# Kernel tuning notes

Measured on AMD Instinct MI355X. Metric: run time of the kernel, lower is better.

## Reference

```python
import jax, jax.numpy as jnp
import numpy as np

TAU = 0.3  # default tau in selectCom_adap
K = 1      # hard-coded K in selectCom_adap

B, C, N, M = 8, 64, 2048, 2048


def setup_inputs() -> dict:
    key = jax.random.key(0)
    k1, k2, k3, k4 = jax.random.split(key, 4)
    return {
        "src_emb": jax.random.normal(k1, (B, C, N), dtype=jnp.float32),
        "tgt_emb": jax.random.normal(k2, (B, C, M), dtype=jnp.float32),
        "src": jax.random.normal(k3, (B, 3, N), dtype=jnp.float32),
        "tgt": jax.random.normal(k4, (B, 3, M), dtype=jnp.float32),
    }


def reference(src_emb, tgt_emb, src, tgt):
    # EPCOR eval path: selectCom_adap + get_sparse_w
    dtype = src_emb.dtype
    Np = src_emb.shape[2]
    Mp = tgt_emb.shape[2]
    tgt_K = int(Mp * TAU)
    src_K = int(Np * TAU)

    inner = jnp.einsum('bcn,bcm->bnm', src_emb, tgt_emb)
    xx = jnp.sum(src_emb * src_emb, axis=1)[:, :, None]   # [B,N,1]
    yy = jnp.sum(tgt_emb * tgt_emb, axis=1)[:, None, :]   # [B,1,M]
    pd = 2.0 * inner - xx - yy                             # [B,N,M]

    # column softmax and tgt outlier mask (smallest tgt_K column mass)
    scoresSoftCol = jax.nn.softmax(pd, axis=2)
    scoresColSum = jnp.sum(scoresSoftCol, axis=1)          # [B,M]
    col_thresh = -jax.lax.top_k(-scoresColSum, tgt_K)[0][:, -1]  # tgt_K-th smallest, [B]
    mask_tgt = (scoresColSum < col_thresh[:, None])[:, None, :]  # [B,1,M]

    # row softmax and src outlier mask (smallest src_K row mass)
    scoresSoftRow = jax.nn.softmax(pd, axis=1)
    scoresRowSum = jnp.sum(scoresSoftRow, axis=2)          # [B,N]
    row_thresh = -jax.lax.top_k(-scoresRowSum, src_K)[0][:, -1]  # [B]
    mask_src = (scoresRowSum < row_thresh[:, None])[:, :, None]  # [B,N,1]

    mask = jnp.logical_or(mask_src, mask_tgt)              # [B,N,M]

    # torch precedence: mask = (mask + scoresSoftCol) < topk  (bool promoted to float)
    topk = jax.lax.top_k(scoresSoftCol, K)[0][..., -1:]    # K-th largest per row, [B,N,1]
    mask = (mask.astype(dtype) + scoresSoftCol) < topk     # [B,N,M]

    w_sparse = jnp.where(mask, jnp.zeros((), dtype), scoresSoftCol)
    colsum = jnp.sum(w_sparse, axis=-1, keepdims=True)
    colsum = jnp.where(colsum < 1e-5, jnp.asarray(1e-5, dtype), colsum)
    src_tgt_weight = w_sparse / colsum                     # row-renormalized sparse weights

    val_sum = jnp.sum(src_tgt_weight, axis=-1, keepdims=True)  # [B,N,1]
    val_sum_inlier = jnp.where(mask_src, jnp.zeros((), dtype), val_sum)[..., 0]  # [B,N]
    src_weight = val_sum_inlier / jnp.sum(val_sum_inlier, axis=-1, keepdims=True)

    # src_corr = tgt @ src_tgt_weight^T : [B,3,M] x [B,N,M] -> [B,3,N]
    src_corr = jnp.einsum('bdm,bnm->bdn', tgt, src_tgt_weight)
    return src_corr, src_weight, mask_src, mask_tgt
```

## Files before the change

### kernel.cpp

```cpp
#include <hip/hip_runtime.h>

#define BB 8
#define CC 64
#define NN 2048
#define MM 2048
#define KSEL 613
#define MT 32
#define MT2 16
#define NT2 16
#define NCH 16

#define OUT_W  (BB * 3 * NN)
#define OUT_MS (OUT_W + BB * NN)
#define OUT_MT (OUT_MS + BB * NN)

typedef __bf16 bf16x8 __attribute__((ext_vector_type(8)));
typedef float f32x4 __attribute__((ext_vector_type(4)));
typedef unsigned short u16;

#define MFMA16 __builtin_amdgcn_mfma_f32_16x16x32_bf16

__device__ __forceinline__ void split3(float a, u16& u0, u16& u1, u16& u2) {
    __bf16 h0 = (__bf16)a; float f0 = (float)h0;
    float r1 = a - f0;
    __bf16 h1 = (__bf16)r1; float f1 = (float)h1;
    float r2 = r1 - f1;
    __bf16 h2 = (__bf16)r2;
    u0 = __builtin_bit_cast(u16, h0);
    u1 = __builtin_bit_cast(u16, h1);
    u2 = __builtin_bit_cast(u16, h2);
}

__global__ __launch_bounds__(256) void split_k(const float* __restrict__ E,
                                               float* __restrict__ sq,
                                               unsigned* __restrict__ T0,
                                               unsigned* __restrict__ T1,
                                               unsigned* __restrict__ T2) {
    __shared__ float Ls[64][65];
    __shared__ float sacc[64];
    int b = blockIdx.y, n0 = blockIdx.x * 64, t = threadIdx.x;
    const float* Eb = E + (size_t)b * CC * NN + n0;
#pragma unroll
    for (int i = 0; i < 4; ++i) {
        int idx = (i << 8) + t, c = idx >> 4, nq = idx & 15;
        float4 v = *(const float4*)(Eb + (size_t)c * NN + (nq << 2));
        Ls[c][nq * 4 + 0] = v.x; Ls[c][nq * 4 + 1] = v.y;
        Ls[c][nq * 4 + 2] = v.z; Ls[c][nq * 4 + 3] = v.w;
    }
    __syncthreads();
    int j = t & 31, nn = t >> 5;
#pragma unroll
    for (int p = 0; p < 8; ++p) {
        int n = (p << 3) + nn;
        float a = Ls[2 * j][n], c = Ls[2 * j + 1][n];
        float s = a * a + c * c;
#pragma unroll
        for (int d = 1; d < 32; d <<= 1) s += __shfl_xor(s, d);
        if (j == 0) sacc[n] = s;
        u16 a0, a1, a2, c0, c1, c2;
        split3(a, a0, a1, a2);
        split3(c, c0, c1, c2);
        size_t row = (size_t)(b * NN + n0 + n) * 32 + j;
        T0[row] = (unsigned)a0 | ((unsigned)c0 << 16);
        T1[row] = (unsigned)a1 | ((unsigned)c1 << 16);
        T2[row] = (unsigned)a2 | ((unsigned)c2 << 16);
    }
    __syncthreads();
    if (t < 64) sq[b * NN + n0 + t] = sacc[t];
}

__device__ __forceinline__ void stage_tile(u16* dst, const unsigned* src,
                                           int base_nm, int kc, int t) {
#pragma unroll
    for (int i = 0; i < 2; ++i) {
        int d = (((i << 8) + t) << 4);
        int nn_ = d >> 6, c4 = (d >> 4) & 3;
        const char* gs = (const char*)src + ((size_t)(base_nm + nn_) << 7) +
                         ((size_t)kc << 6) + ((c4 ^ (nn_ & 3)) << 4);
        __builtin_amdgcn_global_load_lds(
            (const __attribute__((address_space(1))) void*)gs,
            (__attribute__((address_space(3))) void*)((char*)dst + d), 16, 0, 0);
    }
}

__device__ __forceinline__ bf16x8 frag(const u16* tile, int nloc, int g) {
    return *(const bf16x8*)((const char*)tile + (nloc << 6) + ((g ^ (nloc & 3)) << 4));
}

__global__ __launch_bounds__(256, 3) void gemm_pd_k(
    const unsigned* __restrict__ A0, const unsigned* __restrict__ A1, const unsigned* __restrict__ A2,
    const unsigned* __restrict__ B0, const unsigned* __restrict__ B1, const unsigned* __restrict__ B2,
    const float* __restrict__ xx, const float* __restrict__ yy,
    float* __restrict__ pd,
    float* __restrict__ rpM, float* __restrict__ rpS,
    float* __restrict__ cpM, float* __restrict__ cpS) {
    __shared__ u16 Ta0[128 * 32], Tb0[128 * 32], Tax[128 * 32], Tbx[128 * 32];
    __shared__ float rowm2[2][128], rows2[2][128];
    __shared__ float colm2[2][128], cols2[2][128];
    int b = blockIdx.z;
    int n0 = blockIdx.y << 7;
    int m0 = blockIdx.x << 7;
    int t = threadIdx.x, lane = t & 63, w = t >> 6;
    int wn = w >> 1, wm = w & 1;
    int g = lane >> 4, q = lane & 15;
    int baseA = b * NN + n0, baseB = b * MM + m0;

    f32x4 acc[4][4] = {};

#pragma unroll
    for (int kc = 0; kc < 2; ++kc) {
        stage_tile(Ta0, A0, baseA, kc, t);
        stage_tile(Tb0, B0, baseB, kc, t);
        stage_tile(Tax, A1, baseA, kc, t);
        stage_tile(Tbx, B1, baseB, kc, t);
        __syncthreads();
        bf16x8 fa0[4], fb0[4], fax[4], fbx[4];
#pragma unroll
        for (int i = 0; i < 4; ++i) {
            fa0[i] = frag(Ta0, wn * 64 + i * 16 + q, g);
            fb0[i] = frag(Tb0, wm * 64 + i * 16 + q, g);
            fax[i] = frag(Tax, wn * 64 + i * 16 + q, g);
            fbx[i] = frag(Tbx, wm * 64 + i * 16 + q, g);
        }
#pragma unroll
        for (int mg = 0; mg < 4; ++mg)
#pragma unroll
            for (int ng = 0; ng < 4; ++ng)
                acc[ng][mg] = MFMA16(fa0[ng], fb0[mg], acc[ng][mg], 0, 0, 0);
#pragma unroll
        for (int mg = 0; mg < 4; ++mg)
#pragma unroll
            for (int ng = 0; ng < 4; ++ng)
                acc[ng][mg] = MFMA16(fa0[ng], fbx[mg], acc[ng][mg], 0, 0, 0);
#pragma unroll
        for (int mg = 0; mg < 4; ++mg)
#pragma unroll
            for (int ng = 0; ng < 4; ++ng)
                acc[ng][mg] = MFMA16(fax[ng], fb0[mg], acc[ng][mg], 0, 0, 0);
#pragma unroll
        for (int mg = 0; mg < 4; ++mg)
#pragma unroll
            for (int ng = 0; ng < 4; ++ng)
                acc[ng][mg] = MFMA16(fax[ng], fbx[mg], acc[ng][mg], 0, 0, 0);
        __syncthreads();
        stage_tile(Tax, A2, baseA, kc, t);
        stage_tile(Tbx, B2, baseB, kc, t);
        __syncthreads();
#pragma unroll
        for (int i = 0; i < 4; ++i) {
            fax[i] = frag(Tax, wn * 64 + i * 16 + q, g);
            fbx[i] = frag(Tbx, wm * 64 + i * 16 + q, g);
        }
#pragma unroll
        for (int mg = 0; mg < 4; ++mg)
#pragma unroll
            for (int ng = 0; ng < 4; ++ng)
                acc[ng][mg] = MFMA16(fa0[ng], fbx[mg], acc[ng][mg], 0, 0, 0);
#pragma unroll
        for (int mg = 0; mg < 4; ++mg)
#pragma unroll
            for (int ng = 0; ng < 4; ++ng)
                acc[ng][mg] = MFMA16(fax[ng], fb0[mg], acc[ng][mg], 0, 0, 0);
        __syncthreads();
    }

    int nbase = n0 + wn * 64;
    int mbase = m0 + wm * 64;
    float xv[4][4];
#pragma unroll
    for (int ng = 0; ng < 4; ++ng)
#pragma unroll
        for (int r = 0; r < 4; ++r)
            xv[ng][r] = xx[b * NN + nbase + ng * 16 + g * 4 + r];
    float yv[4];
#pragma unroll
    for (int mg = 0; mg < 4; ++mg) yv[mg] = yy[b * MM + mbase + mg * 16 + q];

#pragma unroll
    for (int ng = 0; ng < 4; ++ng)
#pragma unroll
        for (int r = 0; r < 4; ++r) {
            float* prow = pd + ((size_t)(b * NN + nbase + ng * 16 + g * 4 + r)) * MM + mbase + q;
#pragma unroll
            for (int mg = 0; mg < 4; ++mg) {
                float o = 2.f * acc[ng][mg][r] - xv[ng][r] - yv[mg];
                acc[ng][mg][r] = o;
                prow[mg * 16] = o;
            }
        }

#pragma unroll
    for (int ng = 0; ng < 4; ++ng)
#pragma unroll
        for (int r = 0; r < 4; ++r) {
            float mx = fmaxf(fmaxf(acc[ng][0][r], acc[ng][1][r]),
                             fmaxf(acc[ng][2][r], acc[ng][3][r]));
#pragma unroll
            for (int d = 1; d < 16; d <<= 1) mx = fmaxf(mx, __shfl_xor(mx, d));
            float s = __expf(acc[ng][0][r] - mx) + __expf(acc[ng][1][r] - mx) +
                      __expf(acc[ng][2][r] - mx) + __expf(acc[ng][3][r] - mx);
#pragma unroll
            for (int d = 1; d < 16; d <<= 1) s += __shfl_xor(s, d);
            if (q == 0) {
                int nl = wn * 64 + ng * 16 + g * 4 + r;
                rowm2[wm][nl] = mx;
                rows2[wm][nl] = s;
            }
        }

#pragma unroll
    for (int mg = 0; mg < 4; ++mg) {
        float cx = -3.4e38f;
#pragma unroll
        for (int ng = 0; ng < 4; ++ng)
#pragma unroll
            for (int r = 0; r < 4; ++r) cx = fmaxf(cx, acc[ng][mg][r]);
        cx = fmaxf(cx, __shfl_xor(cx, 16));
        cx = fmaxf(cx, __shfl_xor(cx, 32));
        float cs = 0.f;
#pragma unroll
        for (int ng = 0; ng < 4; ++ng)
#pragma unroll
            for (int r = 0; r < 4; ++r) cs += __expf(acc[ng][mg][r] - cx);
        cs += __shfl_xor(cs, 16);
        cs += __shfl_xor(cs, 32);
        if (lane < 16) {
            int ml = wm * 64 + mg * 16 + q;
            colm2[wn][ml] = cx;
            cols2[wn][ml] = cs;
        }
    }
    __syncthreads();

    if (t < 128) {
        float ma = rowm2[0][t], mb = rowm2[1][t];
        float M = fmaxf(ma, mb);
        float S = rows2[0][t] * __expf(ma - M) + rows2[1][t] * __expf(mb - M);
        size_t base = ((size_t)(b * MT2 + blockIdx.x)) * NN + n0 + t;
        rpM[base] = M;
        rpS[base] = S;
    } else {
        int m = t - 128;
        float ma = colm2[0][m], mb = colm2[1][m];
        float M = fmaxf(ma, mb);
        float S = cols2[0][m] * __expf(ma - M) + cols2[1][m] * __expf(mb - M);
        size_t base = ((size_t)(b * NT2 + blockIdx.y)) * MM + m0 + m;
        cpM[base] = M;
        cpS[base] = S;
    }
}

__global__ __launch_bounds__(256) void comb_rc_k(const float* __restrict__ rpM,
                                                 const float* __restrict__ rpS,
                                                 const float* __restrict__ cpM,
                                                 const float* __restrict__ cpS,
                                                 float* __restrict__ rowmax,
                                                 float* __restrict__ rowsum,
                                                 float* __restrict__ colmax,
                                                 float* __restrict__ colsum) {
    int b = blockIdx.y, which = blockIdx.z;
    int i = blockIdx.x * 256 + threadIdx.x;
    const float* pM = which ? cpM : rpM;
    const float* pS = which ? cpS : rpS;
    float* oM = which ? colmax : rowmax;
    float* oS = which ? colsum : rowsum;
    float Mv = -3.4e38f;
#pragma unroll
    for (int k = 0; k < 16; ++k) Mv = fmaxf(Mv, pM[(size_t)(b * 16 + k) * 2048 + i]);
    float S = 0.f;
#pragma unroll
    for (int k = 0; k < 16; ++k) {
        size_t o = (size_t)(b * 16 + k) * 2048 + i;
        S += pS[o] * __expf(pM[o] - Mv);
    }
    oM[b * 2048 + i] = Mv;
    oS[b * 2048 + i] = S;
}

__global__ __launch_bounds__(256) void cross_k(const float* __restrict__ pd,
                                               const float* __restrict__ rowmax,
                                               const float* __restrict__ rowsum,
                                               const float* __restrict__ colmax,
                                               const float* __restrict__ colsum,
                                               float* __restrict__ sRowp,
                                               float* __restrict__ sColp) {
    __shared__ float rmx[128], rin[128];
    __shared__ float rowpart[128][65];
    __shared__ float colacc[4][64];
    int b = blockIdx.z, nc = blockIdx.y, mtile = blockIdx.x;
    int m0 = mtile << 6;
    int t = threadIdx.x, mL = t & 63, ng = t >> 6;
    if (t < 128) {
        int n = nc * 128 + t;
        rmx[t] = rowmax[b * NN + n];
        rin[t] = 1.f / rowsum[b * NN + n];
    }
    float cmv = colmax[b * MM + m0 + mL];
    float civ = 1.f / colsum[b * MM + m0 + mL];
    __syncthreads();
    const float* base = pd + ((size_t)(b * NN + nc * 128)) * MM + m0 + mL;
    float scp = 0.f;
#pragma unroll
    for (int i = 0; i < 32; ++i) {
        int nl = (i << 2) + ng;
        float v = base[(size_t)nl * MM];
        scp += __expf(v - rmx[nl]) * rin[nl];
        rowpart[nl][mL] = __expf(v - cmv) * civ;
    }
    colacc[ng][mL] = scp;
    __syncthreads();
    if (t < 128) {
        float s = 0.f;
#pragma unroll
        for (int c = 0; c < 64; ++c) s += rowpart[t][c];
        sRowp[((size_t)(b * MT + mtile)) * NN + nc * 128 + t] = s;
    } else if (t < 192) {
        int m = t - 128;
        sColp[((size_t)(b * NCH + nc)) * MM + m0 + m] =
            colacc[0][m] + colacc[1][m] + colacc[2][m] + colacc[3][m];
    }
}

__global__ __launch_bounds__(256) void comb_s_k(const float* __restrict__ sRowp,
                                                const float* __restrict__ sColp,
                                                float* __restrict__ sRow,
                                                float* __restrict__ sCol) {
    int b = blockIdx.y, which = blockIdx.z;
    int i = blockIdx.x * 256 + threadIdx.x;
    if (!which) {
        float s = 0.f;
#pragma unroll
        for (int k = 0; k < MT; ++k) s += sRowp[(size_t)(b * MT + k) * NN + i];
        sRow[b * NN + i] = s;
    } else {
        float s = 0.f;
#pragma unroll
        for (int k = 0; k < NCH; ++k) s += sColp[(size_t)(b * NCH + k) * MM + i];
        sCol[b * MM + i] = s;
    }
}

__global__ __launch_bounds__(64) void select_k(const float* __restrict__ sRow,
                                               const float* __restrict__ sCol,
                                               float* __restrict__ rth,
                                               float* __restrict__ cth) {
    int kind = blockIdx.x, b = blockIdx.y, t = threadIdx.x;
    const float* vals = (kind == 0) ? (sRow + b * NN) : (sCol + b * MM);
    float v[32];
#pragma unroll
    for (int i = 0; i < 32; ++i) v[i] = vals[t + (i << 6)];
    unsigned lo = 0u, hi = 0x7F800000u;
    while (lo < hi) {
        unsigned mid = lo + ((hi - lo) >> 1);
        float pv = __uint_as_float(mid);
        int c = 0;
#pragma unroll
        for (int i = 0; i < 32; ++i) c += (v[i] <= pv) ? 1 : 0;
#pragma unroll
        for (int off = 32; off > 0; off >>= 1) c += __shfl_down(c, off);
        c = __shfl(c, 0);
        if (c >= KSEL + 1) hi = mid; else lo = mid + 1;
    }
    if (t == 0) { if (kind == 0) rth[b] = __uint_as_float(lo); else cth[b] = __uint_as_float(lo); }
}

__global__ __launch_bounds__(256) void masks_k(const float* __restrict__ sRow,
                                               const float* __restrict__ sCol,
                                               const float* __restrict__ rth,
                                               const float* __restrict__ cth,
                                               float* __restrict__ out) {
    int b = blockIdx.x, t = threadIdx.x;
    float r = rth[b], c = cth[b];
    int cnt = 0;
    bool ms[8];
#pragma unroll
    for (int i = 0; i < 8; ++i) {
        int n = t + (i << 8);
        ms[i] = sRow[b * NN + n] < r;
        out[OUT_MS + b * NN + n] = ms[i] ? 1.f : 0.f;
        out[OUT_MT + b * MM + n] = (sCol[b * MM + n] < c) ? 1.f : 0.f;
        cnt += ms[i] ? 0 : 1;
    }
#pragma unroll
    for (int off = 32; off > 0; off >>= 1) cnt += __shfl_down(cnt, off);
    __shared__ int wcnt[4];
    int wave = t >> 6, lane = t & 63;
    if (lane == 0) wcnt[wave] = cnt;
    __syncthreads();
    float inv = 1.f / (float)(wcnt[0] + wcnt[1] + wcnt[2] + wcnt[3]);
#pragma unroll
    for (int i = 0; i < 8; ++i) {
        int n = t + (i << 8);
        out[OUT_W + b * NN + n] = ms[i] ? 0.f : inv;
    }
}

__global__ __launch_bounds__(256) void corr_k(const float* __restrict__ pd,
                                              const float* __restrict__ rowmax,
                                              const float* __restrict__ rowsum,
                                              const float* __restrict__ sRow,
                                              const float* __restrict__ sCol,
                                              const float* __restrict__ rth,
                                              const float* __restrict__ cth,
                                              const float* __restrict__ tgt,
                                              float* __restrict__ out) {
    int b = blockIdx.y, n = blockIdx.x, t = threadIdx.x;
    const float4* row4 = (const float4*)(pd + ((size_t)b * NN + n) * MM);
    const float4* sc4 = (const float4*)(sCol + b * MM);
    const float4* tg4 = (const float4*)(tgt + (size_t)b * 3 * MM);
    float rmax = rowmax[b * NN + n];
    float rsum = rowsum[b * NN + n];
    float cthv = cth[b];
    bool msrc = sRow[b * NN + n] < rth[b];
    float cs = 0.f, d0 = 0.f, d1 = 0.f, d2 = 0.f;
#pragma unroll
    for (int g = 0; g < 2; ++g) {
        int j = t + (g << 8);
        float p[4], sc[4], t0[4], t1[4], t2[4];
        *(float4*)p = row4[j];
        *(float4*)sc = sc4[j];
        *(float4*)t0 = tg4[j];
        *(float4*)t1 = tg4[j + MM / 4];
        *(float4*)t2 = tg4[j + MM / 2];
#pragma unroll
        for (int c = 0; c < 4; ++c) {
            bool keep = msrc || (sc[c] < cthv) || (p[c] == rmax);
            if (keep) {
                float s = __expf(p[c] - rmax) / rsum;
                cs += s;
                d0 += s * t0[c];
                d1 += s * t1[c];
                d2 += s * t2[c];
            }
        }
    }
#pragma unroll
    for (int off = 32; off > 0; off >>= 1) {
        cs += __shfl_down(cs, off);
        d0 += __shfl_down(d0, off);
        d1 += __shfl_down(d1, off);
        d2 += __shfl_down(d2, off);
    }
    __shared__ float red[4][4];
    int wave = t >> 6, lane = t & 63;
    if (lane == 0) { red[wave][0] = cs; red[wave][1] = d0; red[wave][2] = d1; red[wave][3] = d2; }
    __syncthreads();
    if (t == 0) {
        float cT = red[0][0] + red[1][0] + red[2][0] + red[3][0];
        float e0 = red[0][1] + red[1][1] + red[2][1] + red[3][1];
        float e1 = red[0][2] + red[1][2] + red[2][2] + red[3][2];
        float e2 = red[0][3] + red[1][3] + red[2][3] + red[3][3];
        cT = (cT < 1e-5f) ? 1e-5f : cT;
        out[(b * 3 + 0) * NN + n] = e0 / cT;
        out[(b * 3 + 1) * NN + n] = e1 / cT;
        out[(b * 3 + 2) * NN + n] = e2 / cT;
    }
}

extern "C" void kernel_launch(void* const* d_in, const int* in_sizes, int n_in,
                              void* d_out, int out_size, void* d_ws, size_t ws_size,
                              hipStream_t stream) {
    const float* src_emb = (const float*)d_in[0];
    const float* tgt_emb = (const float*)d_in[1];
    const float* tgt = (const float*)d_in[3];
    float* out = (float*)d_out;

    float* ws = (float*)d_ws;
    float* pd     = ws;
    float* xx     = pd + (size_t)BB * NN * MM;
    float* yy     = xx + BB * NN;
    float* rowmax = yy + BB * MM;
    float* rowsum = rowmax + BB * NN;
    float* colmax = rowsum + BB * NN;
    float* colsum = colmax + BB * MM;
    float* sRow   = colsum + BB * MM;
    float* sCol   = sRow + BB * NN;
    float* rth    = sCol + BB * MM;
    float* cth    = rth + BB;
    float* rpM    = cth + BB;
    float* rpS    = rpM + (size_t)BB * 16 * NN;
    float* cpM    = rpS + (size_t)BB * 16 * NN;
    float* cpS    = cpM + (size_t)BB * 16 * MM;
    float* sRowp  = cpS + (size_t)BB * 16 * MM;
    float* sColp  = sRowp + (size_t)BB * MT * NN;
    unsigned* At0 = (unsigned*)(sColp + (size_t)BB * NCH * MM);
    unsigned* At1 = At0 + (size_t)BB * NN * 32;
    unsigned* At2 = At1 + (size_t)BB * NN * 32;
    unsigned* Bt0 = At2 + (size_t)BB * NN * 32;
    unsigned* Bt1 = Bt0 + (size_t)BB * MM * 32;
    unsigned* Bt2 = Bt1 + (size_t)BB * MM * 32;

    split_k<<<dim3(NN / 64, BB), 256, 0, stream>>>(src_emb, xx, At0, At1, At2);
    split_k<<<dim3(MM / 64, BB), 256, 0, stream>>>(tgt_emb, yy, Bt0, Bt1, Bt2);
    gemm_pd_k<<<dim3(MM / 128, NN / 128, BB), 256, 0, stream>>>(At0, At1, At2, Bt0, Bt1, Bt2,
                                                                xx, yy, pd, rpM, rpS, cpM, cpS);
    comb_rc_k<<<dim3(2048 / 256, BB, 2), 256, 0, stream>>>(rpM, rpS, cpM, cpS,
                                                           rowmax, rowsum, colmax, colsum);
    cross_k<<<dim3(MT, NCH, BB), 256, 0, stream>>>(pd, rowmax, rowsum, colmax, colsum, sRowp, sColp);
    comb_s_k<<<dim3(2048 / 256, BB, 2), 256, 0, stream>>>(sRowp, sColp, sRow, sCol);
    select_k<<<dim3(2, BB), 64, 0, stream>>>(sRow, sCol, rth, cth);
    masks_k<<<dim3(BB), 256, 0, stream>>>(sRow, sCol, rth, cth, out);
    corr_k<<<dim3(NN, BB), 256, 0, stream>>>(pd, rowmax, rowsum, sRow, sCol, rth, cth, tgt, out);
}
```

Baseline: 203.4 us.

## Load GEMM fragments directly from global memory and remap block indices

```diff
diff --git a/kernel.cpp b/kernel.cpp
--- a/kernel.cpp
+++ b/kernel.cpp
@@ -69,23 +69,7 @@
     if (t < 64) sq[b * NN + n0 + t] = sacc[t];
 }
 
-__device__ __forceinline__ void stage_tile(u16* dst, const unsigned* src,
-                                           int base_nm, int kc, int t) {
-#pragma unroll
-    for (int i = 0; i < 2; ++i) {
-        int d = (((i << 8) + t) << 4);
-        int nn_ = d >> 6, c4 = (d >> 4) & 3;
-        const char* gs = (const char*)src + ((size_t)(base_nm + nn_) << 7) +
-                         ((size_t)kc << 6) + ((c4 ^ (nn_ & 3)) << 4);
-        __builtin_amdgcn_global_load_lds(
-            (const __attribute__((address_space(1))) void*)gs,
-            (__attribute__((address_space(3))) void*)((char*)dst + d), 16, 0, 0);
-    }
-}
-
-__device__ __forceinline__ bf16x8 frag(const u16* tile, int nloc, int g) {
-    return *(const bf16x8*)((const char*)tile + (nloc << 6) + ((g ^ (nloc & 3)) << 4));
-}
+#define LD8(P) (*(const bf16x8*)(const void*)(P))
 
 __global__ __launch_bounds__(256, 3) void gemm_pd_k(
     const unsigned* __restrict__ A0, const unsigned* __restrict__ A1, const unsigned* __restrict__ A2,
@@ -94,74 +78,74 @@
     float* __restrict__ pd,
     float* __restrict__ rpM, float* __restrict__ rpS,
     float* __restrict__ cpM, float* __restrict__ cpS) {
-    __shared__ u16 Ta0[128 * 32], Tb0[128 * 32], Tax[128 * 32], Tbx[128 * 32];
     __shared__ float rowm2[2][128], rows2[2][128];
     __shared__ float colm2[2][128], cols2[2][128];
-    int b = blockIdx.z;
-    int n0 = blockIdx.y << 7;
-    int m0 = blockIdx.x << 7;
+    int flat = blockIdx.x + (blockIdx.y << 4) + (blockIdx.z << 8);
+    int b = flat & 7, rest = flat >> 3;
+    int mt = rest & 15, nt = rest >> 4;
+    int n0 = nt << 7;
+    int m0 = mt << 7;
     int t = threadIdx.x, lane = t & 63, w = t >> 6;
     int wn = w >> 1, wm = w & 1;
     int g = lane >> 4, q = lane & 15;
-    int baseA = b * NN + n0, baseB = b * MM + m0;
+
+    size_t offA = ((size_t)(b * NN + n0 + wn * 64 + q) << 7) + (g << 4);
+    size_t offB = ((size_t)(b * MM + m0 + wm * 64 + q) << 7) + (g << 4);
+    const char* pA0 = (const char*)A0 + offA;
+    const char* pA1 = (const char*)A1 + offA;
+    const char* pA2 = (const char*)A2 + offA;
+    const char* pB0 = (const char*)B0 + offB;
+    const char* pB1 = (const char*)B1 + offB;
+    const char* pB2 = (const char*)B2 + offB;
 
     f32x4 acc[4][4] = {};
 
 #pragma unroll
     for (int kc = 0; kc < 2; ++kc) {
-        stage_tile(Ta0, A0, baseA, kc, t);
-        stage_tile(Tb0, B0, baseB, kc, t);
-        stage_tile(Tax, A1, baseA, kc, t);
-        stage_tile(Tbx, B1, baseB, kc, t);
-        __syncthreads();
-        bf16x8 fa0[4], fb0[4], fax[4], fbx[4];
+        int ko = kc << 6;
+        bf16x8 a0[4], b0[4], ax[4], bx[4];
 #pragma unroll
         for (int i = 0; i < 4; ++i) {
-            fa0[i] = frag(Ta0, wn * 64 + i * 16 + q, g);
-            fb0[i] = frag(Tb0, wm * 64 + i * 16 + q, g);
-            fax[i] = frag(Tax, wn * 64 + i * 16 + q, g);
-            fbx[i] = frag(Tbx, wm * 64 + i * 16 + q, g);
-        }
-#pragma unroll
-        for (int mg = 0; mg < 4; ++mg)
-#pragma unroll
-            for (int ng = 0; ng < 4; ++ng)
-                acc[ng][mg] = MFMA16(fa0[ng], fb0[mg], acc[ng][mg], 0, 0, 0);
-#pragma unroll
-        for (int mg = 0; mg < 4; ++mg)
-#pragma unroll
-            for (int ng = 0; ng < 4; ++ng)
-                acc[ng][mg] = MFMA16(fa0[ng], fbx[mg], acc[ng][mg], 0, 0, 0);
-#pragma unroll
-        for (int mg = 0; mg < 4; ++mg)
-#pragma unroll
-            for (int ng = 0; ng < 4; ++ng)
-                acc[ng][mg] = MFMA16(fax[ng], fb0[mg], acc[ng][mg], 0, 0, 0);
-#pragma unroll
-        for (int mg = 0; mg < 4; ++mg)
-#pragma unroll
-            for (int ng = 0; ng < 4; ++ng)
-                acc[ng][mg] = MFMA16(fax[ng], fbx[mg], acc[ng][mg], 0, 0, 0);
-        __syncthreads();
-        stage_tile(Tax, A2, baseA, kc, t);
-        stage_tile(Tbx, B2, baseB, kc, t);
-        __syncthreads();
+            a0[i] = LD8(pA0 + ko + i * 2048);
+            b0[i] = LD8(pB0 + ko + i * 2048);
+            ax[i] = LD8(pA1 + ko + i * 2048);
+            bx[i] = LD8(pB1 + ko + i * 2048);
+        }
+#pragma unroll
+        for (int mg = 0; mg < 4; ++mg)
+#pragma unroll
+            for (int ng = 0; ng < 4; ++ng)
+                acc[ng][mg] = MFMA16(a0[ng], b0[mg], acc[ng][mg], 0, 0, 0);
+#pragma unroll
+        for (int mg = 0; mg < 4; ++mg)
+#pragma unroll
+            for (int ng = 0; ng < 4; ++ng)
+                acc[ng][mg] = MFMA16(a0[ng], bx[mg], acc[ng][mg], 0, 0, 0);
+#pragma unroll
+        for (int mg = 0; mg < 4; ++mg)
+#pragma unroll
+            for (int ng = 0; ng < 4; ++ng)
+                acc[ng][mg] = MFMA16(ax[ng], b0[mg], acc[ng][mg], 0, 0, 0);
+#pragma unroll
+        for (int mg = 0; mg < 4; ++mg)
+#pragma unroll
+            for (int ng = 0; ng < 4; ++ng)
+                acc[ng][mg] = MFMA16(ax[ng], bx[mg], acc[ng][mg], 0, 0, 0);
 #pragma unroll
         for (int i = 0; i < 4; ++i) {
-            fax[i] = frag(Tax, wn * 64 + i * 16 + q, g);
-            fbx[i] = frag(Tbx, wm * 64 + i * 16 + q, g);
-        }
-#pragma unroll
-        for (int mg = 0; mg < 4; ++mg)
-#pragma unroll
-            for (int ng = 0; ng < 4; ++ng)
-                acc[ng][mg] = MFMA16(fa0[ng], fbx[mg], acc[ng][mg], 0, 0, 0);
-#pragma unroll
-        for (int mg = 0; mg < 4; ++mg)
-#pragma unroll
-            for (int ng = 0; ng < 4; ++ng)
-                acc[ng][mg] = MFMA16(fax[ng], fb0[mg], acc[ng][mg], 0, 0, 0);
-        __syncthreads();
+            ax[i] = LD8(pA2 + ko + i * 2048);
+            bx[i] = LD8(pB2 + ko + i * 2048);
+        }
+#pragma unroll
+        for (int mg = 0; mg < 4; ++mg)
+#pragma unroll
+            for (int ng = 0; ng < 4; ++ng)
+                acc[ng][mg] = MFMA16(a0[ng], bx[mg], acc[ng][mg], 0, 0, 0);
+#pragma unroll
+        for (int mg = 0; mg < 4; ++mg)
+#pragma unroll
+            for (int ng = 0; ng < 4; ++ng)
+                acc[ng][mg] = MFMA16(ax[ng], b0[mg], acc[ng][mg], 0, 0, 0);
     }
 
     int nbase = n0 + wn * 64;
@@ -236,7 +220,7 @@
         float ma = rowm2[0][t], mb = rowm2[1][t];
         float M = fmaxf(ma, mb);
         float S = rows2[0][t] * __expf(ma - M) + rows2[1][t] * __expf(mb - M);
-        size_t base = ((size_t)(b * MT2 + blockIdx.x)) * NN + n0 + t;
+        size_t base = ((size_t)(b * MT2 + mt)) * NN + n0 + t;
         rpM[base] = M;
         rpS[base] = S;
     } else {
@@ -244,7 +228,7 @@
         float ma = colm2[0][m], mb = colm2[1][m];
         float M = fmaxf(ma, mb);
         float S = cols2[0][m] * __expf(ma - M) + cols2[1][m] * __expf(mb - M);
-        size_t base = ((size_t)(b * NT2 + blockIdx.y)) * MM + m0 + m;
+        size_t base = ((size_t)(b * NT2 + nt)) * MM + m0 + m;
         cpM[base] = M;
         cpS[base] = S;
     }
```

Measured after the change: 219.1 us. 1.08x slower.

## Change LDS swizzle, remap GEMM block order by batch, one-wave-per-row corr

Applied to the files above, without the earlier changes.

```diff
diff --git a/kernel.cpp b/kernel.cpp
--- a/kernel.cpp
+++ b/kernel.cpp
@@ -76,7 +76,7 @@
         int d = (((i << 8) + t) << 4);
         int nn_ = d >> 6, c4 = (d >> 4) & 3;
         const char* gs = (const char*)src + ((size_t)(base_nm + nn_) << 7) +
-                         ((size_t)kc << 6) + ((c4 ^ (nn_ & 3)) << 4);
+                         ((size_t)kc << 6) + ((c4 ^ ((nn_ >> 1) & 3)) << 4);
         __builtin_amdgcn_global_load_lds(
             (const __attribute__((address_space(1))) void*)gs,
             (__attribute__((address_space(3))) void*)((char*)dst + d), 16, 0, 0);
@@ -84,7 +84,7 @@
 }
 
 __device__ __forceinline__ bf16x8 frag(const u16* tile, int nloc, int g) {
-    return *(const bf16x8*)((const char*)tile + (nloc << 6) + ((g ^ (nloc & 3)) << 4));
+    return *(const bf16x8*)((const char*)tile + (nloc << 6) + ((g ^ ((nloc >> 1) & 3)) << 4));
 }
 
 __global__ __launch_bounds__(256, 3) void gemm_pd_k(
@@ -97,9 +97,11 @@
     __shared__ u16 Ta0[128 * 32], Tb0[128 * 32], Tax[128 * 32], Tbx[128 * 32];
     __shared__ float rowm2[2][128], rows2[2][128];
     __shared__ float colm2[2][128], cols2[2][128];
-    int b = blockIdx.z;
-    int n0 = blockIdx.y << 7;
-    int m0 = blockIdx.x << 7;
+    int flat = blockIdx.x + (blockIdx.y << 4) + (blockIdx.z << 8);
+    int b = flat & 7, rest = flat >> 3;
+    int mt = rest & 15, nt = rest >> 4;
+    int n0 = nt << 7;
+    int m0 = mt << 7;
     int t = threadIdx.x, lane = t & 63, w = t >> 6;
     int wn = w >> 1, wm = w & 1;
     int g = lane >> 4, q = lane & 15;
@@ -236,7 +238,7 @@
         float ma = rowm2[0][t], mb = rowm2[1][t];
         float M = fmaxf(ma, mb);
         float S = rows2[0][t] * __expf(ma - M) + rows2[1][t] * __expf(mb - M);
-        size_t base = ((size_t)(b * MT2 + blockIdx.x)) * NN + n0 + t;
+        size_t base = ((size_t)(b * MT2 + mt)) * NN + n0 + t;
         rpM[base] = M;
         rpS[base] = S;
     } else {
@@ -244,7 +246,7 @@
         float ma = colm2[0][m], mb = colm2[1][m];
         float M = fmaxf(ma, mb);
         float S = cols2[0][m] * __expf(ma - M) + cols2[1][m] * __expf(mb - M);
-        size_t base = ((size_t)(b * NT2 + blockIdx.y)) * MM + m0 + m;
+        size_t base = ((size_t)(b * NT2 + nt)) * MM + m0 + m;
         cpM[base] = M;
         cpS[base] = S;
     }
@@ -404,7 +406,9 @@
                                               const float* __restrict__ cth,
                                               const float* __restrict__ tgt,
                                               float* __restrict__ out) {
-    int b = blockIdx.y, n = blockIdx.x, t = threadIdx.x;
+    int b = blockIdx.y;
+    int n = (blockIdx.x << 2) + (threadIdx.x >> 6);
+    int lane = threadIdx.x & 63;
     const float4* row4 = (const float4*)(pd + ((size_t)b * NN + n) * MM);
     const float4* sc4 = (const float4*)(sCol + b * MM);
     const float4* tg4 = (const float4*)(tgt + (size_t)b * 3 * MM);
@@ -414,8 +418,8 @@
     bool msrc = sRow[b * NN + n] < rth[b];
     float cs = 0.f, d0 = 0.f, d1 = 0.f, d2 = 0.f;
 #pragma unroll
-    for (int g = 0; g < 2; ++g) {
-        int j = t + (g << 8);
+    for (int g = 0; g < 8; ++g) {
+        int j = lane + (g << 6);
         float p[4], sc[4], t0[4], t1[4], t2[4];
         *(float4*)p = row4[j];
         *(float4*)sc = sc4[j];
@@ -441,19 +445,11 @@
         d1 += __shfl_down(d1, off);
         d2 += __shfl_down(d2, off);
     }
-    __shared__ float red[4][4];
-    int wave = t >> 6, lane = t & 63;
-    if (lane == 0) { red[wave][0] = cs; red[wave][1] = d0; red[wave][2] = d1; red[wave][3] = d2; }
-    __syncthreads();
-    if (t == 0) {
-        float cT = red[0][0] + red[1][0] + red[2][0] + red[3][0];
-        float e0 = red[0][1] + red[1][1] + red[2][1] + red[3][1];
-        float e1 = red[0][2] + red[1][2] + red[2][2] + red[3][2];
-        float e2 = red[0][3] + red[1][3] + red[2][3] + red[3][3];
-        cT = (cT < 1e-5f) ? 1e-5f : cT;
-        out[(b * 3 + 0) * NN + n] = e0 / cT;
-        out[(b * 3 + 1) * NN + n] = e1 / cT;
-        out[(b * 3 + 2) * NN + n] = e2 / cT;
+    if (lane == 0) {
+        cs = (cs < 1e-5f) ? 1e-5f : cs;
+        out[(b * 3 + 0) * NN + n] = d0 / cs;
+        out[(b * 3 + 1) * NN + n] = d1 / cs;
+        out[(b * 3 + 2) * NN + n] = d2 / cs;
     }
 }
 
@@ -492,13 +488,13 @@
 
     split_k<<<dim3(NN / 64, BB), 256, 0, stream>>>(src_emb, xx, At0, At1, At2);
     split_k<<<dim3(MM / 64, BB), 256, 0, stream>>>(tgt_emb, yy, Bt0, Bt1, Bt2);
-    gemm_pd_k<<<dim3(MM / 128, NN / 128, BB), 256, 0, stream>>>(At0, At1, At2, Bt0, Bt1, Bt2,
-                                                                xx, yy, pd, rpM, rpS, cpM, cpS);
+    gemm_pd_k<<<dim3(16, 16, BB), 256, 0, stream>>>(At0, At1, At2, Bt0, Bt1, Bt2,
+                                                    xx, yy, pd, rpM, rpS, cpM, cpS);
     comb_rc_k<<<dim3(2048 / 256, BB, 2), 256, 0, stream>>>(rpM, rpS, cpM, cpS,
                                                            rowmax, rowsum, colmax, colsum);
     cross_k<<<dim3(MT, NCH, BB), 256, 0, stream>>>(pd, rowmax, rowsum, colmax, colsum, sRowp, sColp);
     comb_s_k<<<dim3(2048 / 256, BB, 2), 256, 0, stream>>>(sRowp, sColp, sRow, sCol);
     select_k<<<dim3(2, BB), 64, 0, stream>>>(sRow, sCol, rth, cth);
     masks_k<<<dim3(BB), 256, 0, stream>>>(sRow, sCol, rth, cth, out);
-    corr_k<<<dim3(NN, BB), 256, 0, stream>>>(pd, rowmax, rowsum, sRow, sCol, rth, cth, tgt, out);
-}
+    corr_k<<<dim3(NN / 4, BB), 256, 0, stream>>>(pd, rowmax, rowsum, sRow, sCol, rth, cth, tgt, out);
+}
```

Measured after the change: 195.9 us. 1.04x faster.
